# Performance work log

Hardware: AMD Instinct MI355X
Metric: run time of the kernel (lower is better)

Reference implementation:

```python
import jax, jax.numpy as jnp
import numpy as np

N_NODES = 50000
N_EDGES = 800000
D_IN = 128
D_OUT = 128


def setup_inputs() -> dict:
    key = jax.random.key(0)
    k_x, k_e, k_w, k_b = jax.random.split(key, 4)
    x = jax.random.normal(k_x, (N_NODES, D_IN), dtype=jnp.float32)
    edge_index = jax.random.randint(k_e, (2, N_EDGES), 0, N_NODES, dtype=jnp.int64)
    # nn.Linear(in_dim, out_dim): W is [out, in], b is [out]
    W = jax.random.normal(k_w, (D_OUT, D_IN), dtype=jnp.float32) * (1.0 / np.sqrt(D_IN))
    b = jax.random.normal(k_b, (D_OUT,), dtype=jnp.float32) * 0.01
    return {"x": x, "edge_index": edge_index, "W": W, "b": b}


def reference(x, edge_index, W, b):
    row, col = edge_index[0], edge_index[1]
    n = x.shape[0]
    # scatter-add of gathered source features: agg[row] += x[col]
    agg = jax.ops.segment_sum(x[col], row, num_segments=n)  # [N, d_in]
    # in-degree per destination node (bincount of row), clamped to >= 1
    deg = jax.ops.segment_sum(jnp.ones((row.shape[0],), dtype=x.dtype), row,
                              num_segments=n)
    deg = jnp.maximum(deg, 1.0)[:, None]  # [N, 1]
    agg = agg / deg
    # linear (y = agg @ W.T + b) then relu
    return jax.nn.relu(jnp.einsum('nd,od->no', agg, W) + b)
```

## Files before the change

### kernel.cpp

```cpp
#include <hip/hip_runtime.h>

#define N_NODES 50000
#define N_EDGES 800000
#define D 128

#define NCRS 196
#define CCAP 4608
#define EPB 2048
#define NEBLK ((N_EDGES + EPB - 1) / EPB)
#define NBKT 1563
#define LCAP 1536
#define XN (N_NODES * D / 4)
#define WN (D * D / 4)
#define CBLK ((XN + WN + 255) / 256)

#define XB_OFF   0u
#define WB_OFF   12800000u
#define GCUR_OFF 12832768u
#define CRS_OFF  12833792u
#define WS_NEED_A (CRS_OFF + (unsigned)NCRS * CCAP * 4u)

#define CNT_OFF 0u
#define OFF_OFF 200704u
#define CUR_OFF 401920u
#define CSR_OFF 602112u
#define WT_OFF  3802112u
#define PART_OFF 3867648u
#define BASE_OFF 3868672u
#define WS_NEED_B (BASE_OFF + 1024u)

#define SCAN_B 256
#define SCAN_NBLK ((N_NODES + SCAN_B - 1) / SCAN_B)

using bf16x8 = __attribute__((ext_vector_type(8))) short;
using f32x4 = __attribute__((ext_vector_type(4))) float;

static __device__ __forceinline__ unsigned short bf16_rne(float f) {
  unsigned u = __float_as_uint(f);
  return (unsigned short)((u + 0x7fffu + ((u >> 16) & 1u)) >> 16);
}
static __device__ __forceinline__ unsigned pack_bf16(float a, float b) {
  return (unsigned)bf16_rne(a) | ((unsigned)bf16_rne(b) << 16);
}
static __device__ __forceinline__ float bf_lo(unsigned v) {
  return __uint_as_float(v << 16);
}
static __device__ __forceinline__ float bf_hi(unsigned v) {
  return __uint_as_float(v & 0xffff0000u);
}

__global__ __launch_bounds__(256) void phase1(
    const float4* __restrict__ x4, uint2* __restrict__ xb,
    const float4* __restrict__ w4, uint2* __restrict__ wb,
    const int* __restrict__ ei, unsigned* __restrict__ gcur,
    unsigned* __restrict__ crs) {
  __shared__ unsigned ent[EPB];
  __shared__ unsigned srt[EPB];
  __shared__ unsigned s[256];
  __shared__ unsigned offx[NCRS], cur[NCRS], gb[NCRS];
  const int t = threadIdx.x;

  if (blockIdx.x < NEBLK) {
    const int base = blockIdx.x * EPB;
    const int n = (N_EDGES - base < EPB) ? (N_EDGES - base) : EPB;
    for (int i = t; i < n; i += 256) {
      unsigned dst = (unsigned)ei[base + i];
      unsigned src = (unsigned)ei[N_EDGES + base + i];
      ent[i] = ((dst >> 8) << 24) | (src << 8) | (dst & 255u);
    }
    s[t] = 0;
    __syncthreads();
    for (int i = t; i < n; i += 256) atomicAdd(&s[ent[i] >> 24], 1u);
    __syncthreads();
    unsigned c = s[t];
    __syncthreads();
    s[t] = c;
    __syncthreads();
    #pragma unroll
    for (int o = 1; o < 256; o <<= 1) {
      unsigned a = (t >= o) ? s[t - o] : 0u;
      __syncthreads();
      s[t] += a;
      __syncthreads();
    }
    unsigned ex = s[t] - c;
    if (t < NCRS) {
      offx[t] = ex;
      cur[t] = ex;
      if (c) gb[t] = atomicAdd(&gcur[t], c);
    }
    __syncthreads();
    for (int i = t; i < n; i += 256) {
      unsigned e = ent[i];
      unsigned pos = atomicAdd(&cur[e >> 24], 1u);
      srt[pos] = e;
    }
    __syncthreads();
    for (int i = t; i < n; i += 256) {
      unsigned e = srt[i];
      unsigned k = e >> 24;
      unsigned idx = gb[k] + ((unsigned)i - offx[k]);
      if (idx < CCAP) crs[k * CCAP + idx] = e;
    }
  } else {
    int i = (blockIdx.x - NEBLK) * 256 + t;
    if (i < XN) {
      float4 v = x4[i];
      uint2 r;
      r.x = pack_bf16(v.x, v.y);
      r.y = pack_bf16(v.z, v.w);
      xb[i] = r;
    } else if (i < XN + WN) {
      int j = i - XN;
      float4 v = w4[j];
      uint2 r;
      r.x = pack_bf16(v.x, v.y);
      r.y = pack_bf16(v.z, v.w);
      wb[j] = r;
    }
  }
}

__global__ __launch_bounds__(256) void agg_gemm(
    const unsigned* __restrict__ xb, const unsigned short* __restrict__ wb,
    const unsigned* __restrict__ gcur, const unsigned* __restrict__ crs,
    const float* __restrict__ b, float* __restrict__ out) {
  __shared__ unsigned short lst[LCAP];
  __shared__ unsigned abuf[32 * 64];
  __shared__ unsigned cnt[32], off[32], cur[32];
  const int t = threadIdx.x;
  const int fb = blockIdx.x;
  const int coarse = fb >> 3;
  const unsigned sub = (unsigned)(fb & 7);

  unsigned n = gcur[coarse];
  n = (n > CCAP) ? CCAP : n;
  const unsigned* p = &crs[(unsigned)coarse * CCAP];

  if (t < 32) cnt[t] = 0;
  __syncthreads();
  for (unsigned i = t; i < n; i += 256) {
    unsigned e = p[i];
    if (((e >> 5) & 7u) == sub) atomicAdd(&cnt[e & 31u], 1u);
  }
  __syncthreads();
  if (t < 32) {
    unsigned c = cnt[t], x = c;
    #pragma unroll
    for (int o = 1; o < 32; o <<= 1) {
      unsigned v = __shfl_up(x, o, 64);
      if (t >= o) x += v;
    }
    off[t] = x - c;
    cur[t] = x - c;
  }
  __syncthreads();
  for (unsigned i = t; i < n; i += 256) {
    unsigned e = p[i];
    if (((e >> 5) & 7u) == sub) {
      unsigned pos = atomicAdd(&cur[e & 31u], 1u);
      if (pos < LCAP) lst[pos] = (unsigned short)((e >> 8) & 0xFFFFu);
    }
  }
  __syncthreads();

  const int stream = t >> 5;
  const int p2 = t & 31;
  const uint2* x2 = (const uint2*)xb;
  for (int r = stream; r < 32; r += 8) {
    unsigned beg = off[r], c = cnt[r];
    float a0 = 0.f, a1 = 0.f, a2 = 0.f, a3 = 0.f;
    unsigned j = 0;
    for (; j + 4 <= c; j += 4) {
      unsigned s0 = lst[beg + j], s1 = lst[beg + j + 1];
      unsigned s2 = lst[beg + j + 2], s3 = lst[beg + j + 3];
      uint2 v0 = x2[(size_t)s0 * 32 + p2];
      uint2 v1 = x2[(size_t)s1 * 32 + p2];
      uint2 v2 = x2[(size_t)s2 * 32 + p2];
      uint2 v3 = x2[(size_t)s3 * 32 + p2];
      a0 += bf_lo(v0.x) + bf_lo(v1.x) + bf_lo(v2.x) + bf_lo(v3.x);
      a1 += bf_hi(v0.x) + bf_hi(v1.x) + bf_hi(v2.x) + bf_hi(v3.x);
      a2 += bf_lo(v0.y) + bf_lo(v1.y) + bf_lo(v2.y) + bf_lo(v3.y);
      a3 += bf_hi(v0.y) + bf_hi(v1.y) + bf_hi(v2.y) + bf_hi(v3.y);
    }
    for (; j < c; ++j) {
      uint2 v = x2[(size_t)lst[beg + j] * 32 + p2];
      a0 += bf_lo(v.x);
      a1 += bf_hi(v.x);
      a2 += bf_lo(v.y);
      a3 += bf_hi(v.y);
    }
    float inv = 1.0f / fmaxf((float)c, 1.0f);
    unsigned w0 = (unsigned)(2 * p2) ^ ((unsigned)(r & 7) << 2);
    *(uint2*)&abuf[r * 64 + w0] =
        make_uint2(pack_bf16(a0 * inv, a1 * inv), pack_bf16(a2 * inv, a3 * inv));
  }
  __syncthreads();

  const int wave = t >> 6, lane = t & 63;
  const int rt = wave >> 1;
  const int ch = (wave & 1) * 64;
  const int arow = lane & 15, khi = lane >> 4;
  const int ar = rt * 16 + arow;
  bf16x8 afrag[4];
  #pragma unroll
  for (int kb = 0; kb < 4; ++kb) {
    int w0 = (kb * 16 + khi * 4) ^ ((ar & 7) << 2);
    afrag[kb] = *(const bf16x8*)&abuf[ar * 64 + w0];
  }
  #pragma unroll
  for (int ct = 0; ct < 4; ++ct) {
    int o = ch + ct * 16 + arow;
    f32x4 acc = (f32x4){0.f, 0.f, 0.f, 0.f};
    #pragma unroll
    for (int kb = 0; kb < 4; ++kb) {
      bf16x8 bfrag = *(const bf16x8*)(wb + o * 128 + kb * 32 + khi * 8);
      acc = __builtin_amdgcn_mfma_f32_16x16x32_bf16(afrag[kb], bfrag, acc,
                                                    0, 0, 0);
    }
    float bias = b[o];
    #pragma unroll
    for (int rg = 0; rg < 4; ++rg) {
      int row = fb * 32 + rt * 16 + khi * 4 + rg;
      if (row < N_NODES)
        out[(size_t)row * 128 + o] = fmaxf(acc[rg] + bias, 0.0f);
    }
  }
}

__global__ __launch_bounds__(256) void transpose_w(
    const float* __restrict__ W, float* __restrict__ Wt) {
  int i = blockIdx.x * 256 + threadIdx.x;
  if (i < D * D) {
    int o = i >> 7, d = i & 127;
    Wt[d * D + o] = W[i];
  }
}

__global__ __launch_bounds__(256) void count_kernel(
    const int* __restrict__ ei, unsigned* __restrict__ cnt) {
  int e = blockIdx.x * 256 + threadIdx.x;
  if (e < N_EDGES) atomicAdd(&cnt[ei[e]], 1u);
}

__global__ __launch_bounds__(256) void scan_p1(
    const unsigned* __restrict__ cnt, unsigned* __restrict__ partial) {
  int t = threadIdx.x;
  int g = blockIdx.x * SCAN_B + t;
  unsigned c = (g < N_NODES) ? cnt[g] : 0u;
  #pragma unroll
  for (int o = 32; o > 0; o >>= 1) c += __shfl_down(c, o, 64);
  __shared__ unsigned ws[4];
  if ((t & 63) == 0) ws[t >> 6] = c;
  __syncthreads();
  if (t == 0) partial[blockIdx.x] = ws[0] + ws[1] + ws[2] + ws[3];
}

__global__ __launch_bounds__(256) void scan_p2(
    const unsigned* __restrict__ partial, unsigned* __restrict__ base,
    unsigned* __restrict__ off) {
  __shared__ unsigned s[256];
  int t = threadIdx.x;
  unsigned v = (t < SCAN_NBLK) ? partial[t] : 0u;
  s[t] = v;
  __syncthreads();
  #pragma unroll
  for (int o = 1; o < 256; o <<= 1) {
    unsigned a = (t >= o) ? s[t - o] : 0u;
    __syncthreads();
    s[t] += a;
    __syncthreads();
  }
  if (t < SCAN_NBLK) base[t] = s[t] - v;
  if (t == 255) off[N_NODES] = s[255];
}

__global__ __launch_bounds__(256) void scan_p3(
    const unsigned* __restrict__ cnt, const unsigned* __restrict__ base,
    unsigned* __restrict__ off, unsigned* __restrict__ cur) {
  __shared__ unsigned s[256];
  int t = threadIdx.x;
  int g = blockIdx.x * SCAN_B + t;
  unsigned c = (g < N_NODES) ? cnt[g] : 0u;
  s[t] = c;
  __syncthreads();
  #pragma unroll
  for (int o = 1; o < 256; o <<= 1) {
    unsigned a = (t >= o) ? s[t - o] : 0u;
    __syncthreads();
    s[t] += a;
    __syncthreads();
  }
  if (g < N_NODES) {
    unsigned e = base[blockIdx.x] + s[t] - c;
    off[g] = e;
    cur[g] = e;
  }
}

__global__ __launch_bounds__(256) void fill_kernel(
    const int* __restrict__ ei, unsigned* __restrict__ cur,
    int* __restrict__ csr) {
  int e = blockIdx.x * 256 + threadIdx.x;
  if (e < N_EDGES) {
    int dst = ei[e];
    int src = ei[N_EDGES + e];
    unsigned pos = atomicAdd(&cur[dst], 1u);
    csr[pos] = src;
  }
}

__global__ __launch_bounds__(256) void aggregate_kernel(
    const float* __restrict__ x, const unsigned* __restrict__ off,
    const int* __restrict__ csr, float* __restrict__ agg) {
  int wave = (blockIdx.x * 256 + threadIdx.x) >> 6;
  int lane = threadIdx.x & 63;
  if (wave >= N_NODES) return;
  unsigned beg = off[wave], end = off[wave + 1];
  const float2* x2 = (const float2*)x;
  float ax = 0.f, ay = 0.f;
  unsigned i = beg;
  for (; i + 2 <= end; i += 2) {
    int s0 = csr[i], s1 = csr[i + 1];
    float2 v0 = x2[(size_t)s0 * 64 + lane];
    float2 v1 = x2[(size_t)s1 * 64 + lane];
    ax += v0.x + v1.x;
    ay += v0.y + v1.y;
  }
  if (i < end) {
    float2 v = x2[(size_t)csr[i] * 64 + lane];
    ax += v.x;
    ay += v.y;
  }
  float inv = 1.0f / fmaxf((float)(end - beg), 1.0f);
  float2 r;
  r.x = ax * inv;
  r.y = ay * inv;
  ((float2*)agg)[(size_t)wave * 64 + lane] = r;
}

__global__ __launch_bounds__(256) void gemm_relu_kernel(
    float* __restrict__ io, const float* __restrict__ deg,
    const float* __restrict__ Wt, const float* __restrict__ b) {
  __shared__ float a_lds[32 * 128];
  int tid = threadIdx.x;
  int row0 = blockIdx.x * 32;
  const float4* g4 = (const float4*)io + (size_t)row0 * 32;
  #pragma unroll
  for (int k = 0; k < 4; ++k) {
    int f = k * 256 + tid;
    int r = f >> 5;
    int grow = row0 + r;
    float4 v = make_float4(0.f, 0.f, 0.f, 0.f);
    float inv = 1.0f;
    if (grow < N_NODES) {
      v = g4[f];
      if (deg) inv = 1.0f / fmaxf(deg[grow], 1.0f);
    }
    float* dstp = &a_lds[f * 4];
    dstp[0] = v.x * inv;
    dstp[1] = v.y * inv;
    dstp[2] = v.z * inv;
    dstp[3] = v.w * inv;
  }
  __syncthreads();
  int cq = tid & 31;
  int rb = (tid >> 5) * 4;
  float acc[4][4] = {};
  const float4* Wt4 = (const float4*)Wt;
  #pragma unroll 4
  for (int d = 0; d < 128; ++d) {
    float4 w = Wt4[d * 32 + cq];
    #pragma unroll
    for (int i = 0; i < 4; ++i) {
      float a = a_lds[(rb + i) * 128 + d];
      acc[i][0] += a * w.x;
      acc[i][1] += a * w.y;
      acc[i][2] += a * w.z;
      acc[i][3] += a * w.w;
    }
  }
  float4 bb = ((const float4*)b)[cq];
  float4* out4 = (float4*)io;
  #pragma unroll
  for (int i = 0; i < 4; ++i) {
    int grow = row0 + rb + i;
    if (grow < N_NODES) {
      float4 r;
      r.x = fmaxf(acc[i][0] + bb.x, 0.0f);
      r.y = fmaxf(acc[i][1] + bb.y, 0.0f);
      r.z = fmaxf(acc[i][2] + bb.z, 0.0f);
      r.w = fmaxf(acc[i][3] + bb.w, 0.0f);
      out4[(size_t)grow * 32 + cq] = r;
    }
  }
}

__global__ __launch_bounds__(256) void scatter_kernel(
    const float* __restrict__ x, const int* __restrict__ ei,
    float* __restrict__ agg, float* __restrict__ deg) {
  int gid = blockIdx.x * 256 + threadIdx.x;
  int e = gid >> 5;
  if (e >= N_EDGES) return;
  int part = gid & 31;
  int dst = ei[e];
  int src = ei[N_EDGES + e];
  const float4* x4 = (const float4*)x;
  float4 v = x4[(size_t)src * 32 + part];
  float* base = agg + (size_t)dst * D + part * 4;
  atomicAdd(base + 0, v.x);
  atomicAdd(base + 1, v.y);
  atomicAdd(base + 2, v.z);
  atomicAdd(base + 3, v.w);
  if (part == 0) atomicAdd(deg + dst, 1.0f);
}

extern "C" void kernel_launch(void* const* d_in, const int* in_sizes, int n_in,
                              void* d_out, int out_size, void* d_ws, size_t ws_size,
                              hipStream_t stream) {
  const float* x = (const float*)d_in[0];
  const int* ei = (const int*)d_in[1];
  const float* W = (const float*)d_in[2];
  const float* b = (const float*)d_in[3];
  float* out = (float*)d_out;

  if (ws_size >= WS_NEED_A) {
    unsigned* xb = (unsigned*)((char*)d_ws + XB_OFF);
    unsigned short* wb = (unsigned short*)((char*)d_ws + WB_OFF);
    unsigned* gcur = (unsigned*)((char*)d_ws + GCUR_OFF);
    unsigned* crs = (unsigned*)((char*)d_ws + CRS_OFF);

    hipMemsetAsync(gcur, 0, 1024, stream);
    phase1<<<NEBLK + CBLK, 256, 0, stream>>>(
        (const float4*)x, (uint2*)xb, (const float4*)W, (uint2*)wb,
        ei, gcur, crs);
    agg_gemm<<<NBKT, 256, 0, stream>>>(xb, wb, gcur, crs, b, out);
  } else if (ws_size >= WS_NEED_B) {
    unsigned* cnt = (unsigned*)((char*)d_ws + CNT_OFF);
    unsigned* off = (unsigned*)((char*)d_ws + OFF_OFF);
    unsigned* cur = (unsigned*)((char*)d_ws + CUR_OFF);
    int* csr = (int*)((char*)d_ws + CSR_OFF);
    float* Wt = (float*)((char*)d_ws + WT_OFF);
    unsigned* partial = (unsigned*)((char*)d_ws + PART_OFF);
    unsigned* base = (unsigned*)((char*)d_ws + BASE_OFF);

    hipMemsetAsync(cnt, 0, N_NODES * sizeof(unsigned), stream);
    transpose_w<<<(D * D + 255) / 256, 256, 0, stream>>>(W, Wt);
    count_kernel<<<(N_EDGES + 255) / 256, 256, 0, stream>>>(ei, cnt);
    scan_p1<<<SCAN_NBLK, 256, 0, stream>>>(cnt, partial);
    scan_p2<<<1, 256, 0, stream>>>(partial, base, off);
    scan_p3<<<SCAN_NBLK, 256, 0, stream>>>(cnt, base, off, cur);
    fill_kernel<<<(N_EDGES + 255) / 256, 256, 0, stream>>>(ei, cur, csr);
    aggregate_kernel<<<(N_NODES * 64 + 255) / 256, 256, 0, stream>>>(
        x, off, csr, out);
    gemm_relu_kernel<<<(N_NODES + 31) / 32, 256, 0, stream>>>(
        out, nullptr, Wt, b);
  } else {
    float* deg = (float*)d_ws;
    float* Wt = (float*)((char*)d_ws + 256 * 1024);
    hipMemsetAsync(d_out, 0, (size_t)N_NODES * D * sizeof(float), stream);
    hipMemsetAsync(deg, 0, N_NODES * sizeof(float), stream);
    transpose_w<<<(D * D + 255) / 256, 256, 0, stream>>>(W, Wt);
    scatter_kernel<<<(N_EDGES * 32) / 256, 256, 0, stream>>>(x, ei, out, deg);
    gemm_relu_kernel<<<(N_NODES + 31) / 32, 256, 0, stream>>>(out, deg, Wt, b);
  }
}
```

Before: 76.37 us.

## Split aggregation into feature-sliced gather with pre-sorted bins and separate GEMM

Converts x into eight 16-feature bf16 slices laid out slice-major, so each gather pass touches a 1.6MB slice that can stay cache-resident. A new sortbins kernel sorts each coarse bin once into a per-node CSR in place, replacing the eight-fold redundant rescan of each bin by separate fine blocks. Aggregation is written to a bf16 buffer and a separate MFMA GEMM kernel applies the linear layer, bias and ReLU. This adds two launches and a global round trip for the aggregated features, in exchange for better gather locality and no redundant bin filtering.

```diff
diff --git a/kernel.cpp b/kernel.cpp
--- a/kernel.cpp
+++ b/kernel.cpp
@@ -8,17 +8,19 @@
 #define CCAP 4608
 #define EPB 2048
 #define NEBLK ((N_EDGES + EPB - 1) / EPB)
-#define NBKT 1563
-#define LCAP 1536
-#define XN (N_NODES * D / 4)
+#define NFB 782
+#define NSLC 8
+#define SR (NSLC * N_NODES)
 #define WN (D * D / 4)
-#define CBLK ((XN + WN + 255) / 256)
-
-#define XB_OFF   0u
+#define CVT_ITEMS (SR + WN)
+#define CVTBLK ((CVT_ITEMS + 255) / 256)
+
+#define XS_OFF   0u
 #define WB_OFF   12800000u
 #define GCUR_OFF 12832768u
 #define CRS_OFF  12833792u
-#define WS_NEED_A (CRS_OFF + (unsigned)NCRS * CCAP * 4u)
+#define AGG_OFF  16446464u
+#define WS_NEED_A (AGG_OFF + (unsigned)N_NODES * D * 2u)
 
 #define CNT_OFF 0u
 #define OFF_OFF 200704u
@@ -50,17 +52,17 @@
 }
 
 __global__ __launch_bounds__(256) void phase1(
-    const float4* __restrict__ x4, uint2* __restrict__ xb,
+    const float4* __restrict__ x4, unsigned* __restrict__ xs,
     const float4* __restrict__ w4, uint2* __restrict__ wb,
     const int* __restrict__ ei, unsigned* __restrict__ gcur,
     unsigned* __restrict__ crs) {
-  __shared__ unsigned ent[EPB];
-  __shared__ unsigned srt[EPB];
-  __shared__ unsigned s[256];
-  __shared__ unsigned offx[NCRS], cur[NCRS], gb[NCRS];
   const int t = threadIdx.x;
 
   if (blockIdx.x < NEBLK) {
+    __shared__ unsigned ent[EPB];
+    __shared__ unsigned srt[EPB];
+    __shared__ unsigned s[256];
+    __shared__ unsigned offx[NCRS], cur[NCRS], gb[NCRS];
     const int base = blockIdx.x * EPB;
     const int n = (N_EDGES - base < EPB) ? (N_EDGES - base) : EPB;
     for (int i = t; i < n; i += 256) {
@@ -104,14 +106,25 @@
     }
   } else {
     int i = (blockIdx.x - NEBLK) * 256 + t;
-    if (i < XN) {
-      float4 v = x4[i];
-      uint2 r;
-      r.x = pack_bf16(v.x, v.y);
-      r.y = pack_bf16(v.z, v.w);
-      xb[i] = r;
-    } else if (i < XN + WN) {
-      int j = i - XN;
+    if (i < SR) {
+      int s = i / N_NODES;
+      int node = i - s * N_NODES;
+      const float4* xr = x4 + (size_t)node * 32 + s * 4;
+      float4 f0 = xr[0], f1 = xr[1], f2 = xr[2], f3 = xr[3];
+      uint4 ua, ub;
+      ua.x = pack_bf16(f0.x, f0.y);
+      ua.y = pack_bf16(f0.z, f0.w);
+      ua.z = pack_bf16(f1.x, f1.y);
+      ua.w = pack_bf16(f1.z, f1.w);
+      ub.x = pack_bf16(f2.x, f2.y);
+      ub.y = pack_bf16(f2.z, f2.w);
+      ub.z = pack_bf16(f3.x, f3.y);
+      ub.w = pack_bf16(f3.z, f3.w);
+      uint4* dst = (uint4*)(xs + ((size_t)s * N_NODES + node) * 8);
+      dst[0] = ua;
+      dst[1] = ub;
+    } else if (i < SR + WN) {
+      int j = i - SR;
       float4 v = w4[j];
       uint2 r;
       r.x = pack_bf16(v.x, v.y);
@@ -121,96 +134,111 @@
   }
 }
 
-__global__ __launch_bounds__(256) void agg_gemm(
-    const unsigned* __restrict__ xb, const unsigned short* __restrict__ wb,
-    const unsigned* __restrict__ gcur, const unsigned* __restrict__ crs,
-    const float* __restrict__ b, float* __restrict__ out) {
-  __shared__ unsigned short lst[LCAP];
-  __shared__ unsigned abuf[32 * 64];
-  __shared__ unsigned cnt[32], off[32], cur[32];
+__global__ __launch_bounds__(256) void sortbins(
+    const unsigned* __restrict__ gcur, unsigned* __restrict__ crs) {
+  __shared__ unsigned ent[CCAP];
+  __shared__ unsigned s[256], cur[256];
   const int t = threadIdx.x;
-  const int fb = blockIdx.x;
-  const int coarse = fb >> 3;
-  const unsigned sub = (unsigned)(fb & 7);
-
-  unsigned n = gcur[coarse];
+  const int c = blockIdx.x;
+  unsigned n = gcur[c];
   n = (n > CCAP) ? CCAP : n;
-  const unsigned* p = &crs[(unsigned)coarse * CCAP];
-
-  if (t < 32) cnt[t] = 0;
-  __syncthreads();
+  unsigned* region = crs + (unsigned)c * CCAP;
+
+  for (unsigned i = t; i < n; i += 256) ent[i] = region[i];
+  cur[t] = 0;
+  __syncthreads();
+  for (unsigned i = t; i < n; i += 256) atomicAdd(&cur[ent[i] & 255u], 1u);
+  __syncthreads();
+  unsigned cc = cur[t];
+  __syncthreads();
+  s[t] = cc;
+  __syncthreads();
+  #pragma unroll
+  for (int o = 1; o < 256; o <<= 1) {
+    unsigned a = (t >= o) ? s[t - o] : 0u;
+    __syncthreads();
+    s[t] += a;
+    __syncthreads();
+  }
+  unsigned ex = s[t] - cc;
+  unsigned* offs = region + 2304;
+  offs[t] = ex;
+  if (t == 255) offs[256] = n;
+  cur[t] = ex;
+  __syncthreads();
+  unsigned short* lst = (unsigned short*)region;
   for (unsigned i = t; i < n; i += 256) {
-    unsigned e = p[i];
-    if (((e >> 5) & 7u) == sub) atomicAdd(&cnt[e & 31u], 1u);
-  }
-  __syncthreads();
-  if (t < 32) {
-    unsigned c = cnt[t], x = c;
-    #pragma unroll
-    for (int o = 1; o < 32; o <<= 1) {
-      unsigned v = __shfl_up(x, o, 64);
-      if (t >= o) x += v;
-    }
-    off[t] = x - c;
-    cur[t] = x - c;
-  }
-  __syncthreads();
-  for (unsigned i = t; i < n; i += 256) {
-    unsigned e = p[i];
-    if (((e >> 5) & 7u) == sub) {
-      unsigned pos = atomicAdd(&cur[e & 31u], 1u);
-      if (pos < LCAP) lst[pos] = (unsigned short)((e >> 8) & 0xFFFFu);
-    }
-  }
-  __syncthreads();
-
-  const int stream = t >> 5;
-  const int p2 = t & 31;
-  const uint2* x2 = (const uint2*)xb;
-  for (int r = stream; r < 32; r += 8) {
-    unsigned beg = off[r], c = cnt[r];
-    float a0 = 0.f, a1 = 0.f, a2 = 0.f, a3 = 0.f;
-    unsigned j = 0;
-    for (; j + 4 <= c; j += 4) {
-      unsigned s0 = lst[beg + j], s1 = lst[beg + j + 1];
-      unsigned s2 = lst[beg + j + 2], s3 = lst[beg + j + 3];
-      uint2 v0 = x2[(size_t)s0 * 32 + p2];
-      uint2 v1 = x2[(size_t)s1 * 32 + p2];
-      uint2 v2 = x2[(size_t)s2 * 32 + p2];
-      uint2 v3 = x2[(size_t)s3 * 32 + p2];
-      a0 += bf_lo(v0.x) + bf_lo(v1.x) + bf_lo(v2.x) + bf_lo(v3.x);
-      a1 += bf_hi(v0.x) + bf_hi(v1.x) + bf_hi(v2.x) + bf_hi(v3.x);
-      a2 += bf_lo(v0.y) + bf_lo(v1.y) + bf_lo(v2.y) + bf_lo(v3.y);
-      a3 += bf_hi(v0.y) + bf_hi(v1.y) + bf_hi(v2.y) + bf_hi(v3.y);
-    }
-    for (; j < c; ++j) {
-      uint2 v = x2[(size_t)lst[beg + j] * 32 + p2];
-      a0 += bf_lo(v.x);
-      a1 += bf_hi(v.x);
-      a2 += bf_lo(v.y);
-      a3 += bf_hi(v.y);
-    }
-    float inv = 1.0f / fmaxf((float)c, 1.0f);
-    unsigned w0 = (unsigned)(2 * p2) ^ ((unsigned)(r & 7) << 2);
-    *(uint2*)&abuf[r * 64 + w0] =
-        make_uint2(pack_bf16(a0 * inv, a1 * inv), pack_bf16(a2 * inv, a3 * inv));
-  }
-  __syncthreads();
-
-  const int wave = t >> 6, lane = t & 63;
-  const int rt = wave >> 1;
-  const int ch = (wave & 1) * 64;
-  const int arow = lane & 15, khi = lane >> 4;
-  const int ar = rt * 16 + arow;
+    unsigned e = ent[i];
+    unsigned pos = atomicAdd(&cur[e & 255u], 1u);
+    lst[pos] = (unsigned short)((e >> 8) & 0xFFFFu);
+  }
+}
+
+__global__ __launch_bounds__(256) void agg_slice(
+    const unsigned* __restrict__ xs, const unsigned* __restrict__ crs,
+    unsigned* __restrict__ aggb) {
+  const int t = threadIdx.x;
+  const int fb = blockIdx.x >> 3;
+  const int s = blockIdx.x & 7;
+  const int c = fb >> 2;
+  const int ln0 = (fb & 3) * 64;
+  const int stream = t >> 2;
+  const int p = t & 3;
+  const int nl = ln0 + stream;
+  const int node = c * 256 + nl;
+
+  const unsigned* region = crs + (unsigned)c * CCAP;
+  const unsigned* offs = region + 2304;
+  const unsigned short* lst = (const unsigned short*)region;
+  unsigned beg = offs[nl], end = offs[nl + 1];
+
+  const unsigned* xsl = xs + (size_t)s * (N_NODES * 8);
+  float a0 = 0.f, a1 = 0.f, a2 = 0.f, a3 = 0.f;
+  unsigned j = beg;
+  for (; j + 4 <= end; j += 4) {
+    unsigned s0 = lst[j], s1 = lst[j + 1], s2 = lst[j + 2], s3 = lst[j + 3];
+    uint2 v0 = *(const uint2*)(xsl + s0 * 8 + p * 2);
+    uint2 v1 = *(const uint2*)(xsl + s1 * 8 + p * 2);
+    uint2 v2 = *(const uint2*)(xsl + s2 * 8 + p * 2);
+    uint2 v3 = *(const uint2*)(xsl + s3 * 8 + p * 2);
+    a0 += bf_lo(v0.x) + bf_lo(v1.x) + bf_lo(v2.x) + bf_lo(v3.x);
+    a1 += bf_hi(v0.x) + bf_hi(v1.x) + bf_hi(v2.x) + bf_hi(v3.x);
+    a2 += bf_lo(v0.y) + bf_lo(v1.y) + bf_lo(v2.y) + bf_lo(v3.y);
+    a3 += bf_hi(v0.y) + bf_hi(v1.y) + bf_hi(v2.y) + bf_hi(v3.y);
+  }
+  for (; j < end; ++j) {
+    uint2 v = *(const uint2*)(xsl + lst[j] * 8 + p * 2);
+    a0 += bf_lo(v.x);
+    a1 += bf_hi(v.x);
+    a2 += bf_lo(v.y);
+    a3 += bf_hi(v.y);
+  }
+  float inv = 1.0f / fmaxf((float)(end - beg), 1.0f);
+  if (node < N_NODES) {
+    uint2 r = make_uint2(pack_bf16(a0 * inv, a1 * inv),
+                         pack_bf16(a2 * inv, a3 * inv));
+    *(uint2*)(aggb + (size_t)node * 64 + s * 8 + p * 2) = r;
+  }
+}
+
+__global__ __launch_bounds__(256) void gemm_mfma(
+    const unsigned short* __restrict__ aggb,
+    const unsigned short* __restrict__ wb, const float* __restrict__ b,
+    float* __restrict__ out) {
+  const int wave = threadIdx.x >> 6;
+  const int lane = threadIdx.x & 63;
+  const int row0 = blockIdx.x * 16;
+  const int arow = lane & 15;
+  const int khi = lane >> 4;
+
+  const unsigned short* ap = aggb + (size_t)(row0 + arow) * 128 + khi * 8;
   bf16x8 afrag[4];
   #pragma unroll
-  for (int kb = 0; kb < 4; ++kb) {
-    int w0 = (kb * 16 + khi * 4) ^ ((ar & 7) << 2);
-    afrag[kb] = *(const bf16x8*)&abuf[ar * 64 + w0];
-  }
-  #pragma unroll
-  for (int ct = 0; ct < 4; ++ct) {
-    int o = ch + ct * 16 + arow;
+  for (int kb = 0; kb < 4; ++kb) afrag[kb] = *(const bf16x8*)(ap + kb * 32);
+
+  #pragma unroll
+  for (int ct = 0; ct < 2; ++ct) {
+    int o = wave * 32 + ct * 16 + arow;
     f32x4 acc = (f32x4){0.f, 0.f, 0.f, 0.f};
     #pragma unroll
     for (int kb = 0; kb < 4; ++kb) {
@@ -221,9 +249,8 @@
     float bias = b[o];
     #pragma unroll
     for (int rg = 0; rg < 4; ++rg) {
-      int row = fb * 32 + rt * 16 + khi * 4 + rg;
-      if (row < N_NODES)
-        out[(size_t)row * 128 + o] = fmaxf(acc[rg] + bias, 0.0f);
+      int row = row0 + khi * 4 + rg;
+      out[(size_t)row * 128 + o] = fmaxf(acc[rg] + bias, 0.0f);
     }
   }
 }
@@ -425,16 +452,19 @@
   float* out = (float*)d_out;
 
   if (ws_size >= WS_NEED_A) {
-    unsigned* xb = (unsigned*)((char*)d_ws + XB_OFF);
+    unsigned* xs = (unsigned*)((char*)d_ws + XS_OFF);
     unsigned short* wb = (unsigned short*)((char*)d_ws + WB_OFF);
     unsigned* gcur = (unsigned*)((char*)d_ws + GCUR_OFF);
     unsigned* crs = (unsigned*)((char*)d_ws + CRS_OFF);
+    unsigned* aggb = (unsigned*)((char*)d_ws + AGG_OFF);
 
     hipMemsetAsync(gcur, 0, 1024, stream);
-    phase1<<<NEBLK + CBLK, 256, 0, stream>>>(
-        (const float4*)x, (uint2*)xb, (const float4*)W, (uint2*)wb,
-        ei, gcur, crs);
-    agg_gemm<<<NBKT, 256, 0, stream>>>(xb, wb, gcur, crs, b, out);
+    phase1<<<NEBLK + CVTBLK, 256, 0, stream>>>(
+        (const float4*)x, xs, (const float4*)W, (uint2*)wb, ei, gcur, crs);
+    sortbins<<<NCRS, 256, 0, stream>>>(gcur, crs);
+    agg_slice<<<NFB * NSLC, 256, 0, stream>>>(xs, crs, aggb);
+    gemm_mfma<<<N_NODES / 16, 256, 0, stream>>>(
+        (const unsigned short*)aggb, wb, b, out);
   } else if (ws_size >= WS_NEED_B) {
     unsigned* cnt = (unsigned*)((char*)d_ws + CNT_OFF);
     unsigned* off = (unsigned*)((char*)d_ws + OFF_OFF);
```

Measured after the change: 96.65 us. 1.27x slower.

## Add per-bin counting sort kernel so agg_gemm reads prebuilt CSR lists

Applied to the files above, without the earlier changes.

Adds a sortbins kernel that, once per coarse bin, counting-sorts the edges by destination node and writes a compact uint16 source list plus offsets back into the bin region. agg_gemm then reads its per-row offsets and source lists from global memory instead of having each of the 8 fine blocks rescan the whole coarse bin with LDS atomics. This removes redundant 8x bin scanning and the LCAP truncation in agg_gemm, at the cost of an extra kernel launch and an extra pass over the bin data. It also replaces the memset with a tiny zeroing kernel and scopes phase1's shared arrays to the edge branch.

```diff
diff --git a/kernel.cpp b/kernel.cpp
--- a/kernel.cpp
+++ b/kernel.cpp
@@ -8,11 +8,10 @@
 #define CCAP 4608
 #define EPB 2048
 #define NEBLK ((N_EDGES + EPB - 1) / EPB)
-#define NBKT 1563
-#define LCAP 1536
+#define NFB 1563
 #define XN (N_NODES * D / 4)
 #define WN (D * D / 4)
-#define CBLK ((XN + WN + 255) / 256)
+#define CVTBLK ((XN + WN + 255) / 256)
 
 #define XB_OFF   0u
 #define WB_OFF   12800000u
@@ -49,18 +48,22 @@
   return __uint_as_float(v & 0xffff0000u);
 }
 
+__global__ __launch_bounds__(256) void zero_gcur(unsigned* __restrict__ gcur) {
+  if (threadIdx.x < NCRS) gcur[threadIdx.x] = 0u;
+}
+
 __global__ __launch_bounds__(256) void phase1(
     const float4* __restrict__ x4, uint2* __restrict__ xb,
     const float4* __restrict__ w4, uint2* __restrict__ wb,
     const int* __restrict__ ei, unsigned* __restrict__ gcur,
     unsigned* __restrict__ crs) {
-  __shared__ unsigned ent[EPB];
-  __shared__ unsigned srt[EPB];
-  __shared__ unsigned s[256];
-  __shared__ unsigned offx[NCRS], cur[NCRS], gb[NCRS];
   const int t = threadIdx.x;
 
   if (blockIdx.x < NEBLK) {
+    __shared__ unsigned ent[EPB];
+    __shared__ unsigned srt[EPB];
+    __shared__ unsigned s[256];
+    __shared__ unsigned offx[NCRS], cur[NCRS], gb[NCRS];
     const int base = blockIdx.x * EPB;
     const int n = (N_EDGES - base < EPB) ? (N_EDGES - base) : EPB;
     for (int i = t; i < n; i += 256) {
@@ -121,59 +124,69 @@
   }
 }
 
+__global__ __launch_bounds__(256) void sortbins(
+    const unsigned* __restrict__ gcur, unsigned* __restrict__ crs) {
+  __shared__ unsigned ent[CCAP];
+  __shared__ unsigned s[256], cur[256];
+  const int t = threadIdx.x;
+  const int c = blockIdx.x;
+  unsigned n = gcur[c];
+  n = (n > CCAP) ? CCAP : n;
+  unsigned* region = crs + (unsigned)c * CCAP;
+
+  for (unsigned i = t; i < n; i += 256) ent[i] = region[i];
+  cur[t] = 0;
+  __syncthreads();
+  for (unsigned i = t; i < n; i += 256) atomicAdd(&cur[ent[i] & 255u], 1u);
+  __syncthreads();
+  unsigned cc = cur[t];
+  __syncthreads();
+  s[t] = cc;
+  __syncthreads();
+  #pragma unroll
+  for (int o = 1; o < 256; o <<= 1) {
+    unsigned a = (t >= o) ? s[t - o] : 0u;
+    __syncthreads();
+    s[t] += a;
+    __syncthreads();
+  }
+  unsigned ex = s[t] - cc;
+  unsigned* offs = region + 2304;
+  offs[t] = ex;
+  if (t == 255) offs[256] = n;
+  cur[t] = ex;
+  __syncthreads();
+  unsigned short* lst = (unsigned short*)region;
+  for (unsigned i = t; i < n; i += 256) {
+    unsigned e = ent[i];
+    unsigned pos = atomicAdd(&cur[e & 255u], 1u);
+    lst[pos] = (unsigned short)((e >> 8) & 0xFFFFu);
+  }
+}
+
 __global__ __launch_bounds__(256) void agg_gemm(
     const unsigned* __restrict__ xb, const unsigned short* __restrict__ wb,
-    const unsigned* __restrict__ gcur, const unsigned* __restrict__ crs,
-    const float* __restrict__ b, float* __restrict__ out) {
-  __shared__ unsigned short lst[LCAP];
+    const unsigned* __restrict__ crs, const float* __restrict__ b,
+    float* __restrict__ out) {
   __shared__ unsigned abuf[32 * 64];
-  __shared__ unsigned cnt[32], off[32], cur[32];
   const int t = threadIdx.x;
   const int fb = blockIdx.x;
   const int coarse = fb >> 3;
-  const unsigned sub = (unsigned)(fb & 7);
-
-  unsigned n = gcur[coarse];
-  n = (n > CCAP) ? CCAP : n;
-  const unsigned* p = &crs[(unsigned)coarse * CCAP];
-
-  if (t < 32) cnt[t] = 0;
-  __syncthreads();
-  for (unsigned i = t; i < n; i += 256) {
-    unsigned e = p[i];
-    if (((e >> 5) & 7u) == sub) atomicAdd(&cnt[e & 31u], 1u);
-  }
-  __syncthreads();
-  if (t < 32) {
-    unsigned c = cnt[t], x = c;
-    #pragma unroll
-    for (int o = 1; o < 32; o <<= 1) {
-      unsigned v = __shfl_up(x, o, 64);
-      if (t >= o) x += v;
-    }
-    off[t] = x - c;
-    cur[t] = x - c;
-  }
-  __syncthreads();
-  for (unsigned i = t; i < n; i += 256) {
-    unsigned e = p[i];
-    if (((e >> 5) & 7u) == sub) {
-      unsigned pos = atomicAdd(&cur[e & 31u], 1u);
-      if (pos < LCAP) lst[pos] = (unsigned short)((e >> 8) & 0xFFFFu);
-    }
-  }
-  __syncthreads();
+  const int ln0 = (fb & 7) * 32;
+
+  const unsigned* region = crs + (unsigned)coarse * CCAP;
+  const unsigned* offs = region + 2304;
+  const unsigned short* lst = (const unsigned short*)region;
 
   const int stream = t >> 5;
   const int p2 = t & 31;
   const uint2* x2 = (const uint2*)xb;
   for (int r = stream; r < 32; r += 8) {
-    unsigned beg = off[r], c = cnt[r];
+    unsigned beg = offs[ln0 + r], end = offs[ln0 + r + 1];
     float a0 = 0.f, a1 = 0.f, a2 = 0.f, a3 = 0.f;
-    unsigned j = 0;
-    for (; j + 4 <= c; j += 4) {
-      unsigned s0 = lst[beg + j], s1 = lst[beg + j + 1];
-      unsigned s2 = lst[beg + j + 2], s3 = lst[beg + j + 3];
+    unsigned j = beg;
+    for (; j + 4 <= end; j += 4) {
+      unsigned s0 = lst[j], s1 = lst[j + 1], s2 = lst[j + 2], s3 = lst[j + 3];
       uint2 v0 = x2[(size_t)s0 * 32 + p2];
       uint2 v1 = x2[(size_t)s1 * 32 + p2];
       uint2 v2 = x2[(size_t)s2 * 32 + p2];
@@ -183,14 +196,14 @@
       a2 += bf_lo(v0.y) + bf_lo(v1.y) + bf_lo(v2.y) + bf_lo(v3.y);
       a3 += bf_hi(v0.y) + bf_hi(v1.y) + bf_hi(v2.y) + bf_hi(v3.y);
     }
-    for (; j < c; ++j) {
-      uint2 v = x2[(size_t)lst[beg + j] * 32 + p2];
+    for (; j < end; ++j) {
+      uint2 v = x2[(size_t)lst[j] * 32 + p2];
       a0 += bf_lo(v.x);
       a1 += bf_hi(v.x);
       a2 += bf_lo(v.y);
       a3 += bf_hi(v.y);
     }
-    float inv = 1.0f / fmaxf((float)c, 1.0f);
+    float inv = 1.0f / fmaxf((float)(end - beg), 1.0f);
     unsigned w0 = (unsigned)(2 * p2) ^ ((unsigned)(r & 7) << 2);
     *(uint2*)&abuf[r * 64 + w0] =
         make_uint2(pack_bf16(a0 * inv, a1 * inv), pack_bf16(a2 * inv, a3 * inv));
@@ -430,11 +443,12 @@
     unsigned* gcur = (unsigned*)((char*)d_ws + GCUR_OFF);
     unsigned* crs = (unsigned*)((char*)d_ws + CRS_OFF);
 
-    hipMemsetAsync(gcur, 0, 1024, stream);
-    phase1<<<NEBLK + CBLK, 256, 0, stream>>>(
+    zero_gcur<<<1, 256, 0, stream>>>(gcur);
+    phase1<<<NEBLK + CVTBLK, 256, 0, stream>>>(
         (const float4*)x, (uint2*)xb, (const float4*)W, (uint2*)wb,
         ei, gcur, crs);
-    agg_gemm<<<NBKT, 256, 0, stream>>>(xb, wb, gcur, crs, b, out);
+    sortbins<<<NCRS, 256, 0, stream>>>(gcur, crs);
+    agg_gemm<<<NFB, 256, 0, stream>>>(xb, wb, crs, b, out);
   } else if (ws_size >= WS_NEED_B) {
     unsigned* cnt = (unsigned*)((char*)d_ws + CNT_OFF);
     unsigned* off = (unsigned*)((char*)d_ws + OFF_OFF);
```

New measurement: 79.12 us. +3.6%, slower.
